# Kernel tuning notes

Measured on AMD Instinct MI355X. Metric: run time of the kernel, lower is better.

## Reference

```python
import jax, jax.numpy as jnp
import numpy as np

N, E, F_IN, HID, HEADS, OUT = 50000, 800000, 128, 64, 4, 40


def gat_layer(x, src, dst, n, W, a_src, a_dst, b, heads, ch):
    # PyG GATConv: h = x @ W per head; e_ij = LeakyReLU(a_src.h_j + a_dst.h_i)
    h = (x @ W).reshape(n, heads, ch)
    al_s = jnp.einsum('nhc,hc->nh', h, a_src)  # source-side logit term
    al_d = jnp.einsum('nhc,hc->nh', h, a_dst)  # target-side logit term
    e = jax.nn.leaky_relu(al_s[src] + al_d[dst], negative_slope=0.2)  # [E,H]
    m = jax.ops.segment_max(e, dst, num_segments=n)  # stable softmax per target node
    e = jnp.exp(e - m[dst])
    s = jax.ops.segment_sum(e, dst, num_segments=n)
    alpha = e / s[dst]  # [E,H]
    out = jax.ops.segment_sum(h[src] * alpha[:, :, None], dst, num_segments=n)  # [n,H,C]
    return out.reshape(n, heads * ch) + b


def gat_forward(x, src, dst, W0, as0, ad0, b0, W1, as1, ad1, b1, W2, as2, ad2, b2):
    n = x.shape[0]
    x = jax.nn.elu(gat_layer(x, src, dst, n, W0, as0, ad0, b0, HEADS, HID))
    x = jax.nn.elu(gat_layer(x, src, dst, n, W1, as1, ad1, b1, HEADS, HID))
    x = gat_layer(x, src, dst, n, W2, as2, ad2, b2, 1, OUT)
    return jax.nn.log_softmax(x, axis=1)


def setup_inputs() -> dict:
    key = jax.random.key(0)
    ks = jax.random.split(key, 16)
    x = jax.random.normal(ks[0], (N, F_IN), dtype=jnp.float32)
    edge_index = jax.random.randint(ks[1], (2, E), 0, N, dtype=jnp.int64)
    g = lambda k, sh: jax.random.normal(k, sh, dtype=jnp.float32) * (1.0 / np.sqrt(sh[0]))
    d_hid = HID * HEADS
    return {
        'x': x, 'edge_index': edge_index,
        'W0': g(ks[2], (F_IN, d_hid)), 'as0': g(ks[3], (HEADS, HID)), 'ad0': g(ks[4], (HEADS, HID)), 'b0': jnp.zeros((d_hid,), jnp.float32),
        'W1': g(ks[5], (d_hid, d_hid)), 'as1': g(ks[6], (HEADS, HID)), 'ad1': g(ks[7], (HEADS, HID)), 'b1': jnp.zeros((d_hid,), jnp.float32),
        'W2': g(ks[8], (d_hid, OUT)), 'as2': g(ks[9], (1, OUT)), 'ad2': g(ks[10], (1, OUT)), 'b2': jnp.zeros((OUT,), jnp.float32),
    }


def reference(x, edge_index, W0, as0, ad0, b0, W1, as1, ad1, b1, W2, as2, ad2, b2):
    n = x.shape[0]
    loops = jnp.arange(n, dtype=edge_index.dtype)  # PyG add_self_loops=True
    src = jnp.concatenate([edge_index[0], loops])
    dst = jnp.concatenate([edge_index[1], loops])
    return gat_forward(x, src, dst, W0, as0, ad0, b0, W1, as1, ad1, b1, W2, as2, ad2, b2)
```

## Files before the change

kernel.cpp:

```cpp
#include <hip/hip_runtime.h>
#include <hip/hip_fp16.h>
#include <math.h>

#define NODES 50000
#define NEDGES 800000
#define TOT_E (NEDGES + NODES)
#define SCAN_B 256
#define SCAN_NB ((NODES + SCAN_B - 1) / SCAN_B)

typedef __attribute__((ext_vector_type(8))) _Float16 half8v;
typedef __attribute__((ext_vector_type(4))) float f32x4;

union U2H { uint u; __half2 h; };

static __device__ __forceinline__ float lrelu(float z) {
  return z > 0.f ? z : 0.2f * z;
}
static __device__ __forceinline__ ushort f2h(float f) {
  __half h = __float2half_rn(f);
  return *reinterpret_cast<ushort*>(&h);
}
static __device__ __forceinline__ void wave_lds_fence() {
  __builtin_amdgcn_wave_barrier();
  asm volatile("s_waitcnt lgkmcnt(0)" ::: "memory");
  __builtin_amdgcn_sched_barrier(0);
}

static __device__ __forceinline__ void packB_one(const float* __restrict__ W,
    ushort* __restrict__ Bp, int N, int NF, int idx) {
  int i = idx & 7;
  int lane = (idx >> 3) & 63;
  int rem = idx >> 9;
  int nf = rem % NF;
  int kf = rem / NF;
  int k = kf * 32 + (lane >> 4) * 8 + i;
  int col = nf * 16 + (lane & 15);
  float v = (col < N) ? W[(size_t)k * N + col] : 0.f;
  Bp[idx] = f2h(v);
}

__global__ __launch_bounds__(256) void k_setup(const int* __restrict__ dst,
    int* __restrict__ counts, const float* __restrict__ x, ushort* __restrict__ xb0,
    const float* __restrict__ W0, ushort* __restrict__ Bp0,
    const float* __restrict__ W1, ushort* __restrict__ Bp1,
    const float* __restrict__ W2, ushort* __restrict__ Bp2) {
  int gb = blockIdx.x;
  int tid = threadIdx.x;
  if (gb < 2048) {
    int stride = 2048 * 256;
    for (int i = gb * 256 + tid; i < TOT_E; i += stride) {
      int d = (i < NEDGES) ? dst[i] : (i - NEDGES);
      atomicAdd(&counts[d], 1);
    }
  } else if (gb < 4048) {
    int total4 = NODES * 128 / 4;
    int stride = 2000 * 256;
    for (int i = (gb - 2048) * 256 + tid; i < total4; i += stride) {
      float4 v = *(const float4*)&x[i * 4];
      ushort4 o;
      o.x = f2h(v.x); o.y = f2h(v.y); o.z = f2h(v.z); o.w = f2h(v.w);
      *(ushort4*)&xb0[i * 4] = o;
    }
  } else {
    int b = gb - 4048;
    int stride = 48 * 256;
    int base = b * 256 + tid;
    for (int idx = base; idx < 4 * 16 * 512; idx += stride) packB_one(W0, Bp0, 256, 16, idx);
    for (int idx = base; idx < 8 * 16 * 512; idx += stride) packB_one(W1, Bp1, 256, 16, idx);
    for (int idx = base; idx < 8 * 3 * 512; idx += stride)  packB_one(W2, Bp2, 40, 3, idx);
  }
}

__global__ __launch_bounds__(SCAN_B) void k_scan_red(const int* __restrict__ counts,
                                                     int* __restrict__ bsum) {
  __shared__ int sm[SCAN_B];
  int idx = blockIdx.x * SCAN_B + threadIdx.x;
  int v = (idx < NODES) ? counts[idx] : 0;
  sm[threadIdx.x] = v;
  __syncthreads();
  for (int off = SCAN_B / 2; off > 0; off >>= 1) {
    if (threadIdx.x < off) sm[threadIdx.x] += sm[threadIdx.x + off];
    __syncthreads();
  }
  if (threadIdx.x == 0) bsum[blockIdx.x] = sm[0];
}

__global__ __launch_bounds__(256) void k_scan_part(const int* __restrict__ bsum,
                                                   int* __restrict__ bpre) {
  __shared__ int sm[256];
  int tid = threadIdx.x;
  int v = (tid < SCAN_NB) ? bsum[tid] : 0;
  sm[tid] = v;
  __syncthreads();
  for (int off = 1; off < 256; off <<= 1) {
    int t = (tid >= off) ? sm[tid - off] : 0;
    __syncthreads();
    sm[tid] += t;
    __syncthreads();
  }
  if (tid < SCAN_NB) bpre[tid] = sm[tid] - v;
}

__global__ __launch_bounds__(SCAN_B) void k_scan_emit(const int* __restrict__ counts,
    const int* __restrict__ bpre, int* __restrict__ offs, int* __restrict__ cur) {
  __shared__ int sm[SCAN_B];
  int idx = blockIdx.x * SCAN_B + threadIdx.x;
  int tid = threadIdx.x;
  int v = (idx < NODES) ? counts[idx] : 0;
  sm[tid] = v;
  __syncthreads();
  for (int off = 1; off < SCAN_B; off <<= 1) {
    int t = (tid >= off) ? sm[tid - off] : 0;
    __syncthreads();
    sm[tid] += t;
    __syncthreads();
  }
  int base = bpre[blockIdx.x];
  int excl = base + sm[tid] - v;
  if (idx < NODES) { offs[idx] = excl; cur[idx] = excl; }
  if (idx == NODES - 1) offs[NODES] = excl + v;
}

__global__ void k_scatter(const int* __restrict__ src, const int* __restrict__ dst,
                          int* __restrict__ cur, int* __restrict__ ssrc) {
  int stride = gridDim.x * blockDim.x;
  for (int i = blockIdx.x * blockDim.x + threadIdx.x; i < TOT_E; i += stride) {
    int s, d;
    if (i < NEDGES) { s = src[i]; d = dst[i]; } else { s = i - NEDGES; d = s; }
    int pos = atomicAdd(&cur[d], 1);
    ssrc[pos] = s;
  }
}

template<int KF, int NFW, int CG, int HEADS, int NF_TOT>
__global__ __launch_bounds__(256, 2) void k_gemm_reg(
    const ushort* __restrict__ A, const ushort* __restrict__ Bp,
    ushort* __restrict__ H, const float* __restrict__ a_s, const float* __restrict__ a_d,
    float* __restrict__ al_s, float* __restrict__ al_d, int M, int N, int K) {
  int wib = threadIdx.x >> 6;
  int lane = threadIdx.x & 63;
  int lg = lane >> 4;
  int lr = lane & 15;
  int cg, strip0, sstride;
  if (CG == 4) { cg = wib; strip0 = blockIdx.x; sstride = gridDim.x; }
  else { cg = 0; strip0 = blockIdx.x * 4 + wib; sstride = gridDim.x * 4; }

  half8v b[KF][NFW];
#pragma unroll
  for (int kf = 0; kf < KF; ++kf)
#pragma unroll
    for (int n = 0; n < NFW; ++n)
      b[kf][n] = *(const half8v*)(Bp + ((size_t)(kf * NF_TOT + cg * NFW + n) * 64 + lane) * 8);

  float asc[NFW], adc[NFW];
#pragma unroll
  for (int n = 0; n < NFW; ++n) {
    int col = (cg * NFW + n) * 16 + lr;
    bool ok = col < N;
    asc[n] = ok ? a_s[col] : 0.f;
    adc[n] = ok ? a_d[col] : 0.f;
  }

  int nstrips = M >> 4;
  for (int strip = strip0; strip < nstrips; strip += sstride) {
    const ushort* arow = A + (size_t)(strip * 16 + lr) * K + lg * 8;
    half8v a[KF];
#pragma unroll
    for (int kf = 0; kf < KF; ++kf) a[kf] = *(const half8v*)(arow + kf * 32);
    f32x4 acc[NFW];
#pragma unroll
    for (int n = 0; n < NFW; ++n) acc[n] = (f32x4){0.f, 0.f, 0.f, 0.f};
#pragma unroll
    for (int kf = 0; kf < KF; ++kf)
#pragma unroll
      for (int n = 0; n < NFW; ++n)
        acc[n] = __builtin_amdgcn_mfma_f32_16x16x32_f16(a[kf], b[kf][n], acc[n], 0, 0, 0);

#pragma unroll
    for (int n = 0; n < NFW; ++n) {
      int col = (cg * NFW + n) * 16 + lr;
      if (col < N) {
#pragma unroll
        for (int r = 0; r < 4; ++r) {
          int row = strip * 16 + lg * 4 + r;
          H[(size_t)row * N + col] = f2h(acc[n][r]);
        }
      }
    }

    float ps[4], pd[4];
#pragma unroll
    for (int r = 0; r < 4; ++r) {
      float s = 0.f, d = 0.f;
#pragma unroll
      for (int n = 0; n < NFW; ++n) {
        s += acc[n][r] * asc[n];
        d += acc[n][r] * adc[n];
      }
      ps[r] = s; pd[r] = d;
    }
#pragma unroll
    for (int off = 1; off <= 8; off <<= 1)
#pragma unroll
      for (int t = 0; t < 4; ++t) {
        ps[t] += __shfl_xor(ps[t], off);
        pd[t] += __shfl_xor(pd[t], off);
      }
    if (lr < 4) {
      int row = strip * 16 + lg * 4 + lr;
      if (HEADS == 4) {
        al_s[row * 4 + cg] = ps[lr];
        al_d[row * 4 + cg] = pd[lr];
      } else {
        al_s[row] = ps[lr];
        al_d[row] = pd[lr];
      }
    }
  }
}

__global__ __launch_bounds__(256) void k_agg4(const ushort* __restrict__ hb,
    const float* __restrict__ al_s, const float* __restrict__ al_d,
    const int* __restrict__ offs, const int* __restrict__ ssrc,
    const float* __restrict__ bias, ushort* __restrict__ outb) {
  __shared__ uint s_sv[8][32];
  __shared__ uint s_al[8][4][33];
  int hw = threadIdx.x >> 5;
  int node = (blockIdx.x * 256 + threadIdx.x) >> 5;
  if (node >= NODES) return;
  int l = threadIdx.x & 31;
  int beg = offs[node], end = offs[node + 1];
  float4 ald4 = *(const float4*)&al_d[node * 4];

  float m[4] = {-1e30f, -1e30f, -1e30f, -1e30f};
  for (int i = beg + l; i < end; i += 32) {
    int sv = ssrc[i];
    float4 a4 = *(const float4*)&al_s[sv * 4];
    m[0] = fmaxf(m[0], lrelu(a4.x + ald4.x));
    m[1] = fmaxf(m[1], lrelu(a4.y + ald4.y));
    m[2] = fmaxf(m[2], lrelu(a4.z + ald4.z));
    m[3] = fmaxf(m[3], lrelu(a4.w + ald4.w));
  }
#pragma unroll
  for (int off = 1; off <= 16; off <<= 1) {
#pragma unroll
    for (int h = 0; h < 4; ++h) m[h] = fmaxf(m[h], __shfl_xor(m[h], off));
  }

  int hh = l >> 3;
  uint clb = (uint)l * 8;
  float sacc[4] = {0.f, 0.f, 0.f, 0.f};
  __half2 z2 = __float2half2_rn(0.f);
  __half2 accA[4] = {z2, z2, z2, z2};
  __half2 accB[4] = {z2, z2, z2, z2};

  for (int cb = beg; cb < end; cb += 32) {
    int cnt = min(32, end - cb);
    wave_lds_fence();
    if (l < cnt) {
      uint sv = (uint)ssrc[cb + l];
      float4 a4 = *(const float4*)&al_s[sv * 4];
      float t0 = __expf(lrelu(a4.x + ald4.x) - m[0]);
      float t1 = __expf(lrelu(a4.y + ald4.y) - m[1]);
      float t2 = __expf(lrelu(a4.z + ald4.z) - m[2]);
      float t3 = __expf(lrelu(a4.w + ald4.w) - m[3]);
      sacc[0] += t0; sacc[1] += t1; sacc[2] += t2; sacc[3] += t3;
      U2H p0, p1, p2, p3;
      p0.h = __float2half2_rn(t0); p1.h = __float2half2_rn(t1);
      p2.h = __float2half2_rn(t2); p3.h = __float2half2_rn(t3);
      s_sv[hw][l] = sv;
      s_al[hw][0][l] = p0.u; s_al[hw][1][l] = p1.u;
      s_al[hw][2][l] = p2.u; s_al[hw][3][l] = p3.u;
    }
    wave_lds_fence();
    int e = 0;
    for (; e + 3 < cnt; e += 4) {
      uint sv0 = s_sv[hw][e],     sv1 = s_sv[hw][e + 1];
      uint sv2 = s_sv[hw][e + 2], sv3 = s_sv[hw][e + 3];
      U2H a0, a1, a2, a3;
      a0.u = s_al[hw][hh][e];     a1.u = s_al[hw][hh][e + 1];
      a2.u = s_al[hw][hh][e + 2]; a3.u = s_al[hw][hh][e + 3];
      uint4 hv0 = *(const uint4*)(hb + ((sv0 << 8) + clb));
      uint4 hv1 = *(const uint4*)(hb + ((sv1 << 8) + clb));
      uint4 hv2 = *(const uint4*)(hb + ((sv2 << 8) + clb));
      uint4 hv3 = *(const uint4*)(hb + ((sv3 << 8) + clb));
      U2H v;
      v.u = hv0.x; accA[0] = __hfma2(a0.h, v.h, accA[0]);
      v.u = hv0.y; accA[1] = __hfma2(a0.h, v.h, accA[1]);
      v.u = hv0.z; accA[2] = __hfma2(a0.h, v.h, accA[2]);
      v.u = hv0.w; accA[3] = __hfma2(a0.h, v.h, accA[3]);
      v.u = hv1.x; accB[0] = __hfma2(a1.h, v.h, accB[0]);
      v.u = hv1.y; accB[1] = __hfma2(a1.h, v.h, accB[1]);
      v.u = hv1.z; accB[2] = __hfma2(a1.h, v.h, accB[2]);
      v.u = hv1.w; accB[3] = __hfma2(a1.h, v.h, accB[3]);
      v.u = hv2.x; accA[0] = __hfma2(a2.h, v.h, accA[0]);
      v.u = hv2.y; accA[1] = __hfma2(a2.h, v.h, accA[1]);
      v.u = hv2.z; accA[2] = __hfma2(a2.h, v.h, accA[2]);
      v.u = hv2.w; accA[3] = __hfma2(a2.h, v.h, accA[3]);
      v.u = hv3.x; accB[0] = __hfma2(a3.h, v.h, accB[0]);
      v.u = hv3.y; accB[1] = __hfma2(a3.h, v.h, accB[1]);
      v.u = hv3.z; accB[2] = __hfma2(a3.h, v.h, accB[2]);
      v.u = hv3.w; accB[3] = __hfma2(a3.h, v.h, accB[3]);
    }
    for (; e < cnt; ++e) {
      uint sv = s_sv[hw][e];
      U2H a0; a0.u = s_al[hw][hh][e];
      uint4 hv = *(const uint4*)(hb + ((sv << 8) + clb));
      U2H v;
      v.u = hv.x; accA[0] = __hfma2(a0.h, v.h, accA[0]);
      v.u = hv.y; accA[1] = __hfma2(a0.h, v.h, accA[1]);
      v.u = hv.z; accA[2] = __hfma2(a0.h, v.h, accA[2]);
      v.u = hv.w; accA[3] = __hfma2(a0.h, v.h, accA[3]);
    }
  }
#pragma unroll
  for (int off = 1; off <= 16; off <<= 1) {
#pragma unroll
    for (int h = 0; h < 4; ++h) sacc[h] += __shfl_xor(sacc[h], off);
  }
  float invs = 1.f / sacc[hh];
  ushort4 ores[2];
#pragma unroll
  for (int j = 0; j < 4; ++j) {
    U2H t; t.h = __hadd2(accA[j], accB[j]);
    float lo = __low2float(t.h) * invs + bias[l * 8 + j * 2];
    float hi = __high2float(t.h) * invs + bias[l * 8 + j * 2 + 1];
    lo = lo > 0.f ? lo : __expf(lo) - 1.f;
    hi = hi > 0.f ? hi : __expf(hi) - 1.f;
    ((ushort*)ores)[j * 2]     = f2h(lo);
    ((ushort*)ores)[j * 2 + 1] = f2h(hi);
  }
  *(ushort4*)(outb + (size_t)node * 256 + l * 8)     = ores[0];
  *(ushort4*)(outb + (size_t)node * 256 + l * 8 + 4) = ores[1];
}

__global__ __launch_bounds__(256) void k_agg1(const ushort* __restrict__ hb,
    const float* __restrict__ al_s, const float* __restrict__ al_d,
    const int* __restrict__ offs, const int* __restrict__ ssrc,
    const float* __restrict__ bias, float* __restrict__ out) {
  __shared__ uint s_sv[8][32];
  __shared__ uint s_al[8][32];
  int hw = threadIdx.x >> 5;
  int node = (blockIdx.x * 256 + threadIdx.x) >> 5;
  if (node >= NODES) return;
  int l = threadIdx.x & 31;
  int beg = offs[node], end = offs[node + 1];
  float ald = al_d[node];

  float m = -1e30f;
  for (int i = beg + l; i < end; i += 32)
    m = fmaxf(m, lrelu(al_s[ssrc[i]] + ald));
#pragma unroll
  for (int off = 1; off <= 16; off <<= 1) m = fmaxf(m, __shfl_xor(m, off));

  int p = l >> 4;
  int cq = l & 15;
  bool act = cq < 10;
  uint cqb = (uint)cq * 4;
  float sacc = 0.f;
  __half2 z2 = __float2half2_rn(0.f);
  __half2 accA[2] = {z2, z2};
  __half2 accB[2] = {z2, z2};
  for (int cb = beg; cb < end; cb += 32) {
    int cnt = min(32, end - cb);
    wave_lds_fence();
    if (l < cnt) {
      uint sv = (uint)ssrc[cb + l];
      float t = __expf(lrelu(al_s[sv] + ald) - m);
      sacc += t;
      U2H pk; pk.h = __float2half2_rn(t);
      s_sv[hw][l] = sv;
      s_al[hw][l] = pk.u;
    }
    wave_lds_fence();
    int e = p;
    for (; e + 6 < cnt; e += 8) {
      uint sv0 = s_sv[hw][e],     sv1 = s_sv[hw][e + 2];
      uint sv2 = s_sv[hw][e + 4], sv3 = s_sv[hw][e + 6];
      U2H a0, a1, a2, a3;
      a0.u = s_al[hw][e];     a1.u = s_al[hw][e + 2];
      a2.u = s_al[hw][e + 4]; a3.u = s_al[hw][e + 6];
      if (act) {
        uint2 hv0 = *(const uint2*)(hb + (sv0 * 40u + cqb));
        uint2 hv1 = *(const uint2*)(hb + (sv1 * 40u + cqb));
        uint2 hv2 = *(const uint2*)(hb + (sv2 * 40u + cqb));
        uint2 hv3 = *(const uint2*)(hb + (sv3 * 40u + cqb));
        U2H v;
        v.u = hv0.x; accA[0] = __hfma2(a0.h, v.h, accA[0]);
        v.u = hv0.y; accA[1] = __hfma2(a0.h, v.h, accA[1]);
        v.u = hv1.x; accB[0] = __hfma2(a1.h, v.h, accB[0]);
        v.u = hv1.y; accB[1] = __hfma2(a1.h, v.h, accB[1]);
        v.u = hv2.x; accA[0] = __hfma2(a2.h, v.h, accA[0]);
        v.u = hv2.y; accA[1] = __hfma2(a2.h, v.h, accA[1]);
        v.u = hv3.x; accB[0] = __hfma2(a3.h, v.h, accB[0]);
        v.u = hv3.y; accB[1] = __hfma2(a3.h, v.h, accB[1]);
      }
    }
    for (; e < cnt; e += 2) {
      uint sv = s_sv[hw][e];
      U2H a0; a0.u = s_al[hw][e];
      if (act) {
        uint2 hv = *(const uint2*)(hb + (sv * 40u + cqb));
        U2H v;
        v.u = hv.x; accA[0] = __hfma2(a0.h, v.h, accA[0]);
        v.u = hv.y; accA[1] = __hfma2(a0.h, v.h, accA[1]);
      }
    }
  }
#pragma unroll
  for (int off = 1; off <= 16; off <<= 1) sacc += __shfl_xor(sacc, off);
  float invs = 1.f / sacc;
  float vv[4];
#pragma unroll
  for (int j = 0; j < 2; ++j) {
    U2H t; t.h = __hadd2(accA[j], accB[j]);
    U2H o; o.u = __shfl_xor(t.u, 16);
    t.h = __hadd2(t.h, o.h);
    vv[j * 2]     = __low2float(t.h) * invs;
    vv[j * 2 + 1] = __high2float(t.h) * invs;
  }
  float mm = -1e30f;
  if (act) {
#pragma unroll
    for (int j = 0; j < 4; ++j) {
      vv[j] += bias[cq * 4 + j];
      mm = fmaxf(mm, vv[j]);
    }
  }
#pragma unroll
  for (int off = 1; off <= 8; off <<= 1) mm = fmaxf(mm, __shfl_xor(mm, off));
  float se = 0.f;
  if (act) {
#pragma unroll
    for (int j = 0; j < 4; ++j) se += __expf(vv[j] - mm);
  }
#pragma unroll
  for (int off = 1; off <= 8; off <<= 1) se += __shfl_xor(se, off);
  if (act && p == 0) {
    float lse = mm + __logf(se);
    float4 o;
    o.x = vv[0] - lse; o.y = vv[1] - lse; o.z = vv[2] - lse; o.w = vv[3] - lse;
    *(float4*)&out[(size_t)node * 40 + cq * 4] = o;
  }
}

extern "C" void kernel_launch(void* const* d_in, const int* in_sizes, int n_in,
                              void* d_out, int out_size, void* d_ws, size_t ws_size,
                              hipStream_t stream) {
  const float* x   = (const float*)d_in[0];
  const int*   ei  = (const int*)d_in[1];
  const float* W0  = (const float*)d_in[2];
  const float* as0 = (const float*)d_in[3];
  const float* ad0 = (const float*)d_in[4];
  const float* b0  = (const float*)d_in[5];
  const float* W1  = (const float*)d_in[6];
  const float* as1 = (const float*)d_in[7];
  const float* ad1 = (const float*)d_in[8];
  const float* b1  = (const float*)d_in[9];
  const float* W2  = (const float*)d_in[10];
  const float* as2 = (const float*)d_in[11];
  const float* ad2 = (const float*)d_in[12];
  const float* b2  = (const float*)d_in[13];
  float* out = (float*)d_out;

  char* p = (char*)d_ws;
  auto take = [&](size_t bytes) {
    char* q = p;
    p += (bytes + 255) & ~(size_t)255;
    return (void*)q;
  };
  ushort* xb0 = (ushort*)take((size_t)NODES * 128 * 2);
  ushort* xb1 = (ushort*)take((size_t)NODES * 256 * 2);
  ushort* xb2 = (ushort*)take((size_t)NODES * 256 * 2);
  ushort* hb  = (ushort*)take((size_t)NODES * 256 * 2);
  float* als  = (float*)take((size_t)NODES * 4 * 4);
  float* ald  = (float*)take((size_t)NODES * 4 * 4);
  int* ssrc   = (int*)take((size_t)TOT_E * 4);
  int* offs   = (int*)take((size_t)(NODES + 1) * 4);
  int* cur    = (int*)take((size_t)NODES * 4);
  int* cnt    = (int*)take((size_t)NODES * 4);
  int* bsum   = (int*)take((size_t)SCAN_NB * 4);
  int* bpre   = (int*)take((size_t)SCAN_NB * 4);
  ushort* Bp0 = (ushort*)take((size_t)4 * 16 * 512 * 2);
  ushort* Bp1 = (ushort*)take((size_t)8 * 16 * 512 * 2);
  ushort* Bp2 = (ushort*)take((size_t)8 * 3 * 512 * 2);

  hipMemsetAsync(cnt, 0, (size_t)NODES * 4, stream);
  k_setup<<<4096, 256, 0, stream>>>(ei + NEDGES, cnt, x, xb0, W0, Bp0, W1, Bp1, W2, Bp2);
  k_scan_red<<<SCAN_NB, SCAN_B, 0, stream>>>(cnt, bsum);
  k_scan_part<<<1, 256, 0, stream>>>(bsum, bpre);
  k_scan_emit<<<SCAN_NB, SCAN_B, 0, stream>>>(cnt, bpre, offs, cur);
  k_scatter<<<2048, 256, 0, stream>>>(ei, ei + NEDGES, cur, ssrc);

  int nab = (NODES * 32 + 255) / 256;

  k_gemm_reg<4, 4, 4, 4, 16><<<512, 256, 0, stream>>>(xb0, Bp0, hb, as0, ad0, als, ald, NODES, 256, 128);
  k_agg4<<<nab, 256, 0, stream>>>(hb, als, ald, offs, ssrc, b0, xb1);

  k_gemm_reg<8, 4, 4, 4, 16><<<512, 256, 0, stream>>>(xb1, Bp1, hb, as1, ad1, als, ald, NODES, 256, 256);
  k_agg4<<<nab, 256, 0, stream>>>(hb, als, ald, offs, ssrc, b1, xb2);

  k_gemm_reg<8, 3, 1, 1, 3><<<512, 256, 0, stream>>>(xb2, Bp2, hb, as2, ad2, als, ald, NODES, 40, 256);
  k_agg1<<<nab, 256, 0, stream>>>(hb, als, ald, offs, ssrc, b2, out);
}
```

Measured before the change: 304.3 us.

## Split 4-head aggregation into edge-stats pass and channel-group gather kernel

Replaces the fused per-node aggregation with two kernels. The first computes the softmax max, the per-edge exp weights and the inverse sums, and writes packed (src index | fp16 weight) words per head to a global buffer. The second assigns 16 lanes per node per 32-channel group, spread across 8 blocks, and gathers 4-byte slices of h with nontemporal loads of the packed weights. The aim is more parallelism and no LDS syncs in the gather, at the cost of an extra pass writing about 13.6MB of per-edge data, re-reading the edge list once per channel group, and narrower 4-byte gathers in place of 16-byte ones.

```diff
diff --git a/kernel.cpp b/kernel.cpp
--- a/kernel.cpp
+++ b/kernel.cpp
@@ -219,13 +219,10 @@
   }
 }
 
-__global__ __launch_bounds__(256) void k_agg4(const ushort* __restrict__ hb,
+__global__ __launch_bounds__(256) void k_stats4(
     const float* __restrict__ al_s, const float* __restrict__ al_d,
     const int* __restrict__ offs, const int* __restrict__ ssrc,
-    const float* __restrict__ bias, ushort* __restrict__ outb) {
-  __shared__ uint s_sv[8][32];
-  __shared__ uint s_al[8][4][33];
-  int hw = threadIdx.x >> 5;
+    uint* __restrict__ alp, float* __restrict__ snorm) {
   int node = (blockIdx.x * 256 + threadIdx.x) >> 5;
   if (node >= NODES) return;
   int l = threadIdx.x & 31;
@@ -247,91 +244,84 @@
     for (int h = 0; h < 4; ++h) m[h] = fmaxf(m[h], __shfl_xor(m[h], off));
   }
 
-  int hh = l >> 3;
-  uint clb = (uint)l * 8;
-  float sacc[4] = {0.f, 0.f, 0.f, 0.f};
+  float s0 = 0.f, s1 = 0.f, s2 = 0.f, s3 = 0.f;
+  for (int i = beg + l; i < end; i += 32) {
+    uint sv = (uint)ssrc[i];
+    float4 a4 = *(const float4*)&al_s[sv * 4];
+    float t0 = __expf(lrelu(a4.x + ald4.x) - m[0]);
+    float t1 = __expf(lrelu(a4.y + ald4.y) - m[1]);
+    float t2 = __expf(lrelu(a4.z + ald4.z) - m[2]);
+    float t3 = __expf(lrelu(a4.w + ald4.w) - m[3]);
+    s0 += t0; s1 += t1; s2 += t2; s3 += t3;
+    alp[i]             = sv | ((uint)f2h(t0) << 16);
+    alp[TOT_E + i]     = sv | ((uint)f2h(t1) << 16);
+    alp[2 * TOT_E + i] = sv | ((uint)f2h(t2) << 16);
+    alp[3 * TOT_E + i] = sv | ((uint)f2h(t3) << 16);
+  }
+#pragma unroll
+  for (int off = 1; off <= 16; off <<= 1) {
+    s0 += __shfl_xor(s0, off); s1 += __shfl_xor(s1, off);
+    s2 += __shfl_xor(s2, off); s3 += __shfl_xor(s3, off);
+  }
+  if (l == 0) {
+    float4 inv = make_float4(1.f / s0, 1.f / s1, 1.f / s2, 1.f / s3);
+    *(float4*)&snorm[node * 4] = inv;
+  }
+}
+
+__global__ __launch_bounds__(256) void k_gather4(const ushort* __restrict__ hb,
+    const uint* __restrict__ alp, const float* __restrict__ snorm,
+    const int* __restrict__ offs, const float* __restrict__ bias,
+    ushort* __restrict__ outb) {
+  int bid = blockIdx.x;
+  int cg = bid & 7;
+  int chunk = bid >> 3;
+  int g = threadIdx.x >> 4;
+  int l = threadIdx.x & 15;
+  int node = chunk * 16 + g;
+  if (node >= NODES) return;
+  int beg = offs[node], end = offs[node + 1];
+  int hh = cg >> 1;
+  const uint* alph = alp + (size_t)hh * TOT_E;
+  uint choff = ((uint)cg << 5) + ((uint)l << 1);
+
   __half2 z2 = __float2half2_rn(0.f);
-  __half2 accA[4] = {z2, z2, z2, z2};
-  __half2 accB[4] = {z2, z2, z2, z2};
-
-  for (int cb = beg; cb < end; cb += 32) {
-    int cnt = min(32, end - cb);
-    wave_lds_fence();
-    if (l < cnt) {
-      uint sv = (uint)ssrc[cb + l];
-      float4 a4 = *(const float4*)&al_s[sv * 4];
-      float t0 = __expf(lrelu(a4.x + ald4.x) - m[0]);
-      float t1 = __expf(lrelu(a4.y + ald4.y) - m[1]);
-      float t2 = __expf(lrelu(a4.z + ald4.z) - m[2]);
-      float t3 = __expf(lrelu(a4.w + ald4.w) - m[3]);
-      sacc[0] += t0; sacc[1] += t1; sacc[2] += t2; sacc[3] += t3;
-      U2H p0, p1, p2, p3;
-      p0.h = __float2half2_rn(t0); p1.h = __float2half2_rn(t1);
-      p2.h = __float2half2_rn(t2); p3.h = __float2half2_rn(t3);
-      s_sv[hw][l] = sv;
-      s_al[hw][0][l] = p0.u; s_al[hw][1][l] = p1.u;
-      s_al[hw][2][l] = p2.u; s_al[hw][3][l] = p3.u;
-    }
-    wave_lds_fence();
-    int e = 0;
-    for (; e + 3 < cnt; e += 4) {
-      uint sv0 = s_sv[hw][e],     sv1 = s_sv[hw][e + 1];
-      uint sv2 = s_sv[hw][e + 2], sv3 = s_sv[hw][e + 3];
-      U2H a0, a1, a2, a3;
-      a0.u = s_al[hw][hh][e];     a1.u = s_al[hw][hh][e + 1];
-      a2.u = s_al[hw][hh][e + 2]; a3.u = s_al[hw][hh][e + 3];
-      uint4 hv0 = *(const uint4*)(hb + ((sv0 << 8) + clb));
-      uint4 hv1 = *(const uint4*)(hb + ((sv1 << 8) + clb));
-      uint4 hv2 = *(const uint4*)(hb + ((sv2 << 8) + clb));
-      uint4 hv3 = *(const uint4*)(hb + ((sv3 << 8) + clb));
-      U2H v;
-      v.u = hv0.x; accA[0] = __hfma2(a0.h, v.h, accA[0]);
-      v.u = hv0.y; accA[1] = __hfma2(a0.h, v.h, accA[1]);
-      v.u = hv0.z; accA[2] = __hfma2(a0.h, v.h, accA[2]);
-      v.u = hv0.w; accA[3] = __hfma2(a0.h, v.h, accA[3]);
-      v.u = hv1.x; accB[0] = __hfma2(a1.h, v.h, accB[0]);
-      v.u = hv1.y; accB[1] = __hfma2(a1.h, v.h, accB[1]);
-      v.u = hv1.z; accB[2] = __hfma2(a1.h, v.h, accB[2]);
-      v.u = hv1.w; accB[3] = __hfma2(a1.h, v.h, accB[3]);
-      v.u = hv2.x; accA[0] = __hfma2(a2.h, v.h, accA[0]);
-      v.u = hv2.y; accA[1] = __hfma2(a2.h, v.h, accA[1]);
-      v.u = hv2.z; accA[2] = __hfma2(a2.h, v.h, accA[2]);
-      v.u = hv2.w; accA[3] = __hfma2(a2.h, v.h, accA[3]);
-      v.u = hv3.x; accB[0] = __hfma2(a3.h, v.h, accB[0]);
-      v.u = hv3.y; accB[1] = __hfma2(a3.h, v.h, accB[1]);
-      v.u = hv3.z; accB[2] = __hfma2(a3.h, v.h, accB[2]);
-      v.u = hv3.w; accB[3] = __hfma2(a3.h, v.h, accB[3]);
-    }
-    for (; e < cnt; ++e) {
-      uint sv = s_sv[hw][e];
-      U2H a0; a0.u = s_al[hw][hh][e];
-      uint4 hv = *(const uint4*)(hb + ((sv << 8) + clb));
-      U2H v;
-      v.u = hv.x; accA[0] = __hfma2(a0.h, v.h, accA[0]);
-      v.u = hv.y; accA[1] = __hfma2(a0.h, v.h, accA[1]);
-      v.u = hv.z; accA[2] = __hfma2(a0.h, v.h, accA[2]);
-      v.u = hv.w; accA[3] = __hfma2(a0.h, v.h, accA[3]);
-    }
-  }
-#pragma unroll
-  for (int off = 1; off <= 16; off <<= 1) {
-#pragma unroll
-    for (int h = 0; h < 4; ++h) sacc[h] += __shfl_xor(sacc[h], off);
-  }
-  float invs = 1.f / sacc[hh];
-  ushort4 ores[2];
-#pragma unroll
-  for (int j = 0; j < 4; ++j) {
-    U2H t; t.h = __hadd2(accA[j], accB[j]);
-    float lo = __low2float(t.h) * invs + bias[l * 8 + j * 2];
-    float hi = __high2float(t.h) * invs + bias[l * 8 + j * 2 + 1];
-    lo = lo > 0.f ? lo : __expf(lo) - 1.f;
-    hi = hi > 0.f ? hi : __expf(hi) - 1.f;
-    ((ushort*)ores)[j * 2]     = f2h(lo);
-    ((ushort*)ores)[j * 2 + 1] = f2h(hi);
-  }
-  *(ushort4*)(outb + (size_t)node * 256 + l * 8)     = ores[0];
-  *(ushort4*)(outb + (size_t)node * 256 + l * 8 + 4) = ores[1];
+  __half2 accA = z2, accB = z2;
+  int i = beg;
+  for (; i + 3 < end; i += 4) {
+    uint u0 = __builtin_nontemporal_load(&alph[i]);
+    uint u1 = __builtin_nontemporal_load(&alph[i + 1]);
+    uint u2 = __builtin_nontemporal_load(&alph[i + 2]);
+    uint u3 = __builtin_nontemporal_load(&alph[i + 3]);
+    U2H v0, v1, v2, v3;
+    v0.u = *(const uint*)(hb + (((u0 & 0xFFFFu) << 8) + choff));
+    v1.u = *(const uint*)(hb + (((u1 & 0xFFFFu) << 8) + choff));
+    v2.u = *(const uint*)(hb + (((u2 & 0xFFFFu) << 8) + choff));
+    v3.u = *(const uint*)(hb + (((u3 & 0xFFFFu) << 8) + choff));
+    U2H a0, a1, a2, a3;
+    a0.u = (u0 >> 16) * 0x10001u;
+    a1.u = (u1 >> 16) * 0x10001u;
+    a2.u = (u2 >> 16) * 0x10001u;
+    a3.u = (u3 >> 16) * 0x10001u;
+    accA = __hfma2(a0.h, v0.h, accA);
+    accB = __hfma2(a1.h, v1.h, accB);
+    accA = __hfma2(a2.h, v2.h, accA);
+    accB = __hfma2(a3.h, v3.h, accB);
+  }
+  for (; i < end; ++i) {
+    uint u = __builtin_nontemporal_load(&alph[i]);
+    U2H v; v.u = *(const uint*)(hb + (((u & 0xFFFFu) << 8) + choff));
+    U2H a; a.u = (u >> 16) * 0x10001u;
+    accA = __hfma2(a.h, v.h, accA);
+  }
+  __half2 acc = __hadd2(accA, accB);
+  float invs = snorm[node * 4 + hh];
+  float lo = __low2float(acc) * invs + bias[(cg << 5) + l * 2];
+  float hi = __high2float(acc) * invs + bias[(cg << 5) + l * 2 + 1];
+  lo = lo > 0.f ? lo : __expf(lo) - 1.f;
+  hi = hi > 0.f ? hi : __expf(hi) - 1.f;
+  ushort2 o = make_ushort2(f2h(lo), f2h(hi));
+  *(ushort2*)(outb + (size_t)node * 256 + choff) = o;
 }
 
 __global__ __launch_bounds__(256) void k_agg1(const ushort* __restrict__ hb,
@@ -475,7 +465,9 @@
   ushort* hb  = (ushort*)take((size_t)NODES * 256 * 2);
   float* als  = (float*)take((size_t)NODES * 4 * 4);
   float* ald  = (float*)take((size_t)NODES * 4 * 4);
+  float* snorm= (float*)take((size_t)NODES * 4 * 4);
   int* ssrc   = (int*)take((size_t)TOT_E * 4);
+  uint* alp   = (uint*)take((size_t)4 * TOT_E * 4);
   int* offs   = (int*)take((size_t)(NODES + 1) * 4);
   int* cur    = (int*)take((size_t)NODES * 4);
   int* cnt    = (int*)take((size_t)NODES * 4);
@@ -492,14 +484,17 @@
   k_scan_emit<<<SCAN_NB, SCAN_B, 0, stream>>>(cnt, bpre, offs, cur);
   k_scatter<<<2048, 256, 0, stream>>>(ei, ei + NEDGES, cur, ssrc);
 
-  int nab = (NODES * 32 + 255) / 256;
+  int nsb = (NODES * 32 + 255) / 256;
+  int ngb = (NODES / 16) * 8;
 
   k_gemm_reg<4, 4, 4, 4, 16><<<512, 256, 0, stream>>>(xb0, Bp0, hb, as0, ad0, als, ald, NODES, 256, 128);
-  k_agg4<<<nab, 256, 0, stream>>>(hb, als, ald, offs, ssrc, b0, xb1);
+  k_stats4<<<nsb, 256, 0, stream>>>(als, ald, offs, ssrc, alp, snorm);
+  k_gather4<<<ngb, 256, 0, stream>>>(hb, alp, snorm, offs, b0, xb1);
 
   k_gemm_reg<8, 4, 4, 4, 16><<<512, 256, 0, stream>>>(xb1, Bp1, hb, as1, ad1, als, ald, NODES, 256, 256);
-  k_agg4<<<nab, 256, 0, stream>>>(hb, als, ald, offs, ssrc, b1, xb2);
+  k_stats4<<<nsb, 256, 0, stream>>>(als, ald, offs, ssrc, alp, snorm);
+  k_gather4<<<ngb, 256, 0, stream>>>(hb, alp, snorm, offs, b1, xb2);
 
   k_gemm_reg<8, 3, 1, 1, 3><<<512, 256, 0, stream>>>(xb2, Bp2, hb, as2, ad2, als, ald, NODES, 40, 256);
-  k_agg1<<<nab, 256, 0, stream>>>(hb, als, ald, offs, ssrc, b2, out);
-}
+  k_agg1<<<nsb, 256, 0, stream>>>(hb, als, ald, offs, ssrc, b2, out);
+}
```

New measurement: 467.9 us. +53.8%, slower.

## Aggregate raw features before projection in layer 0; fold attention vectors into W0

Applied to the files above, without the earlier changes.

Layer 0 now precomputes W0·a_src and W0·a_dst so the attention logits come straight from the 128-wide fp16 input. The per-head weighted aggregation then runs over 128-wide raw features instead of 256-wide projected ones, followed by a per-head MFMA GEMM that applies 1/sum normalisation, bias and ELU. This reorders aggregation and the linear map, which is valid because the map is linear. Separately, the scan reduce and partial-scan kernels merge through a last-block atomic, the logit computation is fused into the scan-emit launch, and the CSR source indices shrink to 16-bit. The GEMM in layer 0 now processes per-head aggregates (512 wide per node), so its work grows while the gather traffic shrinks.

```diff
diff --git a/kernel.cpp b/kernel.cpp
--- a/kernel.cpp
+++ b/kernel.cpp
@@ -7,6 +7,7 @@
 #define TOT_E (NEDGES + NODES)
 #define SCAN_B 256
 #define SCAN_NB ((NODES + SCAN_B - 1) / SCAN_B)
+#define ALOG_NB (NODES / 16)
 
 typedef __attribute__((ext_vector_type(8))) _Float16 half8v;
 typedef __attribute__((ext_vector_type(4))) float f32x4;
@@ -41,7 +42,9 @@
 
 __global__ __launch_bounds__(256) void k_setup(const int* __restrict__ dst,
     int* __restrict__ counts, const float* __restrict__ x, ushort* __restrict__ xb0,
-    const float* __restrict__ W0, ushort* __restrict__ Bp0,
+    const float* __restrict__ W0, ushort* __restrict__ Bq0,
+    float* __restrict__ Uu, float* __restrict__ Vv,
+    const float* __restrict__ as0, const float* __restrict__ ad0,
     const float* __restrict__ W1, ushort* __restrict__ Bp1,
     const float* __restrict__ W2, ushort* __restrict__ Bp2) {
   int gb = blockIdx.x;
@@ -61,19 +64,47 @@
       o.x = f2h(v.x); o.y = f2h(v.y); o.z = f2h(v.z); o.w = f2h(v.w);
       *(ushort4*)&xb0[i * 4] = o;
     }
-  } else {
+  } else if (gb < 4096) {
     int b = gb - 4048;
     int stride = 48 * 256;
     int base = b * 256 + tid;
-    for (int idx = base; idx < 4 * 16 * 512; idx += stride) packB_one(W0, Bp0, 256, 16, idx);
     for (int idx = base; idx < 8 * 16 * 512; idx += stride) packB_one(W1, Bp1, 256, 16, idx);
     for (int idx = base; idx < 8 * 3 * 512; idx += stride)  packB_one(W2, Bp2, 40, 3, idx);
-  }
-}
-
-__global__ __launch_bounds__(SCAN_B) void k_scan_red(const int* __restrict__ counts,
-                                                     int* __restrict__ bsum) {
+  } else if (gb < 4224) {
+    int idx = (gb - 4096) * 256 + tid;
+    int i = idx & 7;
+    int lane = (idx >> 3) & 63;
+    int rem = idx >> 9;
+    int nf = rem & 3;
+    int kf = (rem >> 2) & 3;
+    int h = rem >> 4;
+    int k = kf * 32 + (lane >> 4) * 8 + i;
+    int col = h * 64 + nf * 16 + (lane & 15);
+    Bq0[idx] = f2h(W0[(size_t)k * 256 + col]);
+  } else {
+    int idx = (gb - 4224) * 256 + tid;
+    if (idx < 512) {
+      int c = idx & 127;
+      int h = idx >> 7;
+      float su = 0.f, sv = 0.f;
+      const float* wr = &W0[(size_t)c * 256 + h * 64];
+      const float* ar = &as0[h * 64];
+      const float* dr = &ad0[h * 64];
+#pragma unroll 8
+      for (int j = 0; j < 64; ++j) {
+        su += wr[j] * ar[j];
+        sv += wr[j] * dr[j];
+      }
+      Uu[c * 4 + h] = su;
+      Vv[c * 4 + h] = sv;
+    }
+  }
+}
+
+__global__ __launch_bounds__(SCAN_B) void k_scan_red_part(const int* __restrict__ counts,
+    int* __restrict__ bsum, int* __restrict__ bpre, int* __restrict__ done) {
   __shared__ int sm[SCAN_B];
+  __shared__ int lastflag;
   int idx = blockIdx.x * SCAN_B + threadIdx.x;
   int v = (idx < NODES) ? counts[idx] : 0;
   sm[threadIdx.x] = v;
@@ -82,53 +113,245 @@
     if (threadIdx.x < off) sm[threadIdx.x] += sm[threadIdx.x + off];
     __syncthreads();
   }
-  if (threadIdx.x == 0) bsum[blockIdx.x] = sm[0];
-}
-
-__global__ __launch_bounds__(256) void k_scan_part(const int* __restrict__ bsum,
-                                                   int* __restrict__ bpre) {
-  __shared__ int sm[256];
+  if (threadIdx.x == 0) {
+    __hip_atomic_store(&bsum[blockIdx.x], sm[0], __ATOMIC_RELEASE, __HIP_MEMORY_SCOPE_AGENT);
+    int t = __hip_atomic_fetch_add(done, 1, __ATOMIC_ACQ_REL, __HIP_MEMORY_SCOPE_AGENT);
+    lastflag = (t == (int)gridDim.x - 1);
+  }
+  __syncthreads();
+  if (!lastflag) return;
   int tid = threadIdx.x;
-  int v = (tid < SCAN_NB) ? bsum[tid] : 0;
-  sm[tid] = v;
+  int b = (tid < SCAN_NB)
+      ? __hip_atomic_load(&bsum[tid], __ATOMIC_ACQUIRE, __HIP_MEMORY_SCOPE_AGENT) : 0;
+  __syncthreads();
+  sm[tid] = b;
   __syncthreads();
   for (int off = 1; off < 256; off <<= 1) {
-    int t = (tid >= off) ? sm[tid - off] : 0;
+    int t2 = (tid >= off) ? sm[tid - off] : 0;
     __syncthreads();
-    sm[tid] += t;
+    sm[tid] += t2;
     __syncthreads();
   }
-  if (tid < SCAN_NB) bpre[tid] = sm[tid] - v;
-}
-
-__global__ __launch_bounds__(SCAN_B) void k_scan_emit(const int* __restrict__ counts,
-    const int* __restrict__ bpre, int* __restrict__ offs, int* __restrict__ cur) {
-  __shared__ int sm[SCAN_B];
-  int idx = blockIdx.x * SCAN_B + threadIdx.x;
-  int tid = threadIdx.x;
-  int v = (idx < NODES) ? counts[idx] : 0;
-  sm[tid] = v;
-  __syncthreads();
-  for (int off = 1; off < SCAN_B; off <<= 1) {
-    int t = (tid >= off) ? sm[tid - off] : 0;
+  if (tid < SCAN_NB) bpre[tid] = sm[tid] - b;
+}
+
+__global__ __launch_bounds__(SCAN_B) void k_scan_emit_alog(const int* __restrict__ counts,
+    const int* __restrict__ bpre, int* __restrict__ offs, int* __restrict__ cur,
+    const ushort* __restrict__ xb0, const float* __restrict__ Uu,
+    const float* __restrict__ Vv, float* __restrict__ als, float* __restrict__ ald) {
+  if (blockIdx.x < SCAN_NB) {
+    __shared__ int sm[SCAN_B];
+    int idx = blockIdx.x * SCAN_B + threadIdx.x;
+    int tid = threadIdx.x;
+    int v = (idx < NODES) ? counts[idx] : 0;
+    sm[tid] = v;
     __syncthreads();
-    sm[tid] += t;
-    __syncthreads();
-  }
-  int base = bpre[blockIdx.x];
-  int excl = base + sm[tid] - v;
-  if (idx < NODES) { offs[idx] = excl; cur[idx] = excl; }
-  if (idx == NODES - 1) offs[NODES] = excl + v;
+    for (int off = 1; off < SCAN_B; off <<= 1) {
+      int t = (tid >= off) ? sm[tid - off] : 0;
+      __syncthreads();
+      sm[tid] += t;
+      __syncthreads();
+    }
+    int base = bpre[blockIdx.x];
+    int excl = base + sm[tid] - v;
+    if (idx < NODES) { offs[idx] = excl; cur[idx] = excl; }
+    if (idx == NODES - 1) offs[NODES] = excl + v;
+    return;
+  }
+  int node = ((blockIdx.x - SCAN_NB) * 256 + threadIdx.x) >> 4;
+  int l = threadIdx.x & 15;
+  float s4[4] = {0.f, 0.f, 0.f, 0.f};
+  float d4[4] = {0.f, 0.f, 0.f, 0.f};
+  uint4 raw = *(const uint4*)(xb0 + (size_t)node * 128 + l * 8);
+  const uint* rw = &raw.x;
+#pragma unroll
+  for (int w = 0; w < 4; ++w) {
+    U2H u; u.u = rw[w];
+    float x0 = __low2float(u.h), x1 = __high2float(u.h);
+    int c0 = l * 8 + w * 2;
+    float4 u0 = *(const float4*)&Uu[c0 * 4];
+    float4 u1 = *(const float4*)&Uu[(c0 + 1) * 4];
+    float4 v0 = *(const float4*)&Vv[c0 * 4];
+    float4 v1 = *(const float4*)&Vv[(c0 + 1) * 4];
+    s4[0] += x0 * u0.x + x1 * u1.x; s4[1] += x0 * u0.y + x1 * u1.y;
+    s4[2] += x0 * u0.z + x1 * u1.z; s4[3] += x0 * u0.w + x1 * u1.w;
+    d4[0] += x0 * v0.x + x1 * v1.x; d4[1] += x0 * v0.y + x1 * v1.y;
+    d4[2] += x0 * v0.z + x1 * v1.z; d4[3] += x0 * v0.w + x1 * v1.w;
+  }
+#pragma unroll
+  for (int off = 1; off <= 8; off <<= 1) {
+#pragma unroll
+    for (int h = 0; h < 4; ++h) {
+      s4[h] += __shfl_xor(s4[h], off);
+      d4[h] += __shfl_xor(d4[h], off);
+    }
+  }
+  if (l == 0) {
+    *(float4*)&als[node * 4] = make_float4(s4[0], s4[1], s4[2], s4[3]);
+    *(float4*)&ald[node * 4] = make_float4(d4[0], d4[1], d4[2], d4[3]);
+  }
 }
 
 __global__ void k_scatter(const int* __restrict__ src, const int* __restrict__ dst,
-                          int* __restrict__ cur, int* __restrict__ ssrc) {
+                          int* __restrict__ cur, ushort* __restrict__ ssrc) {
   int stride = gridDim.x * blockDim.x;
   for (int i = blockIdx.x * blockDim.x + threadIdx.x; i < TOT_E; i += stride) {
     int s, d;
     if (i < NEDGES) { s = src[i]; d = dst[i]; } else { s = i - NEDGES; d = s; }
     int pos = atomicAdd(&cur[d], 1);
-    ssrc[pos] = s;
+    ssrc[pos] = (ushort)s;
+  }
+}
+
+__global__ __launch_bounds__(256) void k_agg0(const ushort* __restrict__ xb0,
+    const float* __restrict__ al_s, const float* __restrict__ al_d,
+    const int* __restrict__ offs, const ushort* __restrict__ ssrc,
+    ushort* __restrict__ agg, float* __restrict__ snorm) {
+  __shared__ uint s_sv[8][32];
+  __shared__ uint2 s_al2[8][32];
+  int hw = threadIdx.x >> 5;
+  int node = (blockIdx.x * 256 + threadIdx.x) >> 5;
+  if (node >= NODES) return;
+  int l = threadIdx.x & 31;
+  int beg = offs[node], end = offs[node + 1];
+  float4 ald4 = *(const float4*)&al_d[node * 4];
+
+  float m[4] = {-1e30f, -1e30f, -1e30f, -1e30f};
+  for (int i = beg + l; i < end; i += 32) {
+    int sv = ssrc[i];
+    float4 a4 = *(const float4*)&al_s[sv * 4];
+    m[0] = fmaxf(m[0], lrelu(a4.x + ald4.x));
+    m[1] = fmaxf(m[1], lrelu(a4.y + ald4.y));
+    m[2] = fmaxf(m[2], lrelu(a4.z + ald4.z));
+    m[3] = fmaxf(m[3], lrelu(a4.w + ald4.w));
+  }
+#pragma unroll
+  for (int off = 1; off <= 16; off <<= 1) {
+#pragma unroll
+    for (int h = 0; h < 4; ++h) m[h] = fmaxf(m[h], __shfl_xor(m[h], off));
+  }
+
+  float sacc[4] = {0.f, 0.f, 0.f, 0.f};
+  __half2 z2 = __float2half2_rn(0.f);
+  __half2 accA[8] = {z2, z2, z2, z2, z2, z2, z2, z2};
+  __half2 accB[8] = {z2, z2, z2, z2, z2, z2, z2, z2};
+  uint clb = (uint)l * 4;
+
+  for (int cb = beg; cb < end; cb += 32) {
+    int cnt = min(32, end - cb);
+    wave_lds_fence();
+    if (l < cnt) {
+      uint sv = (uint)ssrc[cb + l];
+      float4 a4 = *(const float4*)&al_s[sv * 4];
+      float t0 = __expf(lrelu(a4.x + ald4.x) - m[0]);
+      float t1 = __expf(lrelu(a4.y + ald4.y) - m[1]);
+      float t2 = __expf(lrelu(a4.z + ald4.z) - m[2]);
+      float t3 = __expf(lrelu(a4.w + ald4.w) - m[3]);
+      sacc[0] += t0; sacc[1] += t1; sacc[2] += t2; sacc[3] += t3;
+      s_sv[hw][l] = sv;
+      s_al2[hw][l] = make_uint2((uint)f2h(t0) | ((uint)f2h(t1) << 16),
+                                (uint)f2h(t2) | ((uint)f2h(t3) << 16));
+    }
+    wave_lds_fence();
+    int e = 0;
+    for (; e + 3 < cnt; e += 4) {
+      uint sv0 = s_sv[hw][e],     sv1 = s_sv[hw][e + 1];
+      uint sv2 = s_sv[hw][e + 2], sv3 = s_sv[hw][e + 3];
+      uint2 w0 = s_al2[hw][e],     w1 = s_al2[hw][e + 1];
+      uint2 w2 = s_al2[hw][e + 2], w3 = s_al2[hw][e + 3];
+      uint2 hv0 = *(const uint2*)(xb0 + ((sv0 << 7) + clb));
+      uint2 hv1 = *(const uint2*)(xb0 + ((sv1 << 7) + clb));
+      uint2 hv2 = *(const uint2*)(xb0 + ((sv2 << 7) + clb));
+      uint2 hv3 = *(const uint2*)(xb0 + ((sv3 << 7) + clb));
+      U2H a, v;
+#define EDGE(ACC, W, HV)                                                      \
+      v.u = HV.x;                                                             \
+      a.u = (W.x & 0xFFFFu) * 0x10001u; ACC[0] = __hfma2(a.h, v.h, ACC[0]);   \
+      a.u = (W.x >> 16) * 0x10001u;     ACC[2] = __hfma2(a.h, v.h, ACC[2]);   \
+      a.u = (W.y & 0xFFFFu) * 0x10001u; ACC[4] = __hfma2(a.h, v.h, ACC[4]);   \
+      a.u = (W.y >> 16) * 0x10001u;     ACC[6] = __hfma2(a.h, v.h, ACC[6]);   \
+      v.u = HV.y;                                                             \
+      a.u = (W.x & 0xFFFFu) * 0x10001u; ACC[1] = __hfma2(a.h, v.h, ACC[1]);   \
+      a.u = (W.x >> 16) * 0x10001u;     ACC[3] = __hfma2(a.h, v.h, ACC[3]);   \
+      a.u = (W.y & 0xFFFFu) * 0x10001u; ACC[5] = __hfma2(a.h, v.h, ACC[5]);   \
+      a.u = (W.y >> 16) * 0x10001u;     ACC[7] = __hfma2(a.h, v.h, ACC[7]);
+      EDGE(accA, w0, hv0)
+      EDGE(accB, w1, hv1)
+      EDGE(accA, w2, hv2)
+      EDGE(accB, w3, hv3)
+    }
+    for (; e < cnt; ++e) {
+      uint sv = s_sv[hw][e];
+      uint2 w = s_al2[hw][e];
+      uint2 hv = *(const uint2*)(xb0 + ((sv << 7) + clb));
+      U2H a, v;
+      EDGE(accA, w, hv)
+    }
+#undef EDGE
+  }
+#pragma unroll
+  for (int off = 1; off <= 16; off <<= 1) {
+#pragma unroll
+    for (int h = 0; h < 4; ++h) sacc[h] += __shfl_xor(sacc[h], off);
+  }
+  if (l == 0) {
+    *(float4*)&snorm[node * 4] = make_float4(1.f / sacc[0], 1.f / sacc[1],
+                                             1.f / sacc[2], 1.f / sacc[3]);
+  }
+#pragma unroll
+  for (int h = 0; h < 4; ++h) {
+    U2H a0, a1;
+    a0.h = __hadd2(accA[h * 2], accB[h * 2]);
+    a1.h = __hadd2(accA[h * 2 + 1], accB[h * 2 + 1]);
+    *(uint2*)(agg + (size_t)node * 512 + h * 128 + clb) = make_uint2(a0.u, a1.u);
+  }
+}
+
+__global__ __launch_bounds__(256, 2) void k_gemm_post(const ushort* __restrict__ agg,
+    const ushort* __restrict__ Bq0, const float* __restrict__ snorm,
+    const float* __restrict__ bias, ushort* __restrict__ xb1) {
+  int h = threadIdx.x >> 6;
+  int lane = threadIdx.x & 63;
+  int lg = lane >> 4;
+  int lr = lane & 15;
+
+  half8v b[4][4];
+#pragma unroll
+  for (int kf = 0; kf < 4; ++kf)
+#pragma unroll
+    for (int n = 0; n < 4; ++n)
+      b[kf][n] = *(const half8v*)(Bq0 + (((size_t)(h * 4 + kf) * 4 + n) * 64 + lane) * 8);
+
+  int nstrips = NODES >> 4;
+  for (int strip = blockIdx.x; strip < nstrips; strip += gridDim.x) {
+    const ushort* arow = agg + (size_t)(strip * 16 + lr) * 512 + h * 128 + lg * 8;
+    half8v a[4];
+#pragma unroll
+    for (int kf = 0; kf < 4; ++kf) a[kf] = *(const half8v*)(arow + kf * 32);
+    f32x4 acc[4];
+#pragma unroll
+    for (int n = 0; n < 4; ++n) acc[n] = (f32x4){0.f, 0.f, 0.f, 0.f};
+#pragma unroll
+    for (int kf = 0; kf < 4; ++kf)
+#pragma unroll
+      for (int n = 0; n < 4; ++n)
+        acc[n] = __builtin_amdgcn_mfma_f32_16x16x32_f16(a[kf], b[kf][n], acc[n], 0, 0, 0);
+
+    float sn[4];
+#pragma unroll
+    for (int r = 0; r < 4; ++r) sn[r] = snorm[(strip * 16 + lg * 4 + r) * 4 + h];
+#pragma unroll
+    for (int n = 0; n < 4; ++n) {
+      int col = h * 64 + n * 16 + lr;
+      float bcol = bias[col];
+#pragma unroll
+      for (int r = 0; r < 4; ++r) {
+        int node = strip * 16 + lg * 4 + r;
+        float v = acc[n][r] * sn[r] + bcol;
+        v = v > 0.f ? v : __expf(v) - 1.f;
+        xb1[(size_t)node * 256 + col] = f2h(v);
+      }
+    }
   }
 }
 
@@ -221,7 +444,7 @@
 
 __global__ __launch_bounds__(256) void k_agg4(const ushort* __restrict__ hb,
     const float* __restrict__ al_s, const float* __restrict__ al_d,
-    const int* __restrict__ offs, const int* __restrict__ ssrc,
+    const int* __restrict__ offs, const ushort* __restrict__ ssrc,
     const float* __restrict__ bias, ushort* __restrict__ outb) {
   __shared__ uint s_sv[8][32];
   __shared__ uint s_al[8][4][33];
@@ -336,7 +559,7 @@
 
 __global__ __launch_bounds__(256) void k_agg1(const ushort* __restrict__ hb,
     const float* __restrict__ al_s, const float* __restrict__ al_d,
-    const int* __restrict__ offs, const int* __restrict__ ssrc,
+    const int* __restrict__ offs, const ushort* __restrict__ ssrc,
     const float* __restrict__ bias, float* __restrict__ out) {
   __shared__ uint s_sv[8][32];
   __shared__ uint s_al[8][32];
@@ -473,29 +696,35 @@
   ushort* xb1 = (ushort*)take((size_t)NODES * 256 * 2);
   ushort* xb2 = (ushort*)take((size_t)NODES * 256 * 2);
   ushort* hb  = (ushort*)take((size_t)NODES * 256 * 2);
+  ushort* agg = xb2;
   float* als  = (float*)take((size_t)NODES * 4 * 4);
   float* ald  = (float*)take((size_t)NODES * 4 * 4);
-  int* ssrc   = (int*)take((size_t)TOT_E * 4);
+  float* snorm= (float*)take((size_t)NODES * 4 * 4);
+  ushort* ssrc= (ushort*)take((size_t)TOT_E * 2);
   int* offs   = (int*)take((size_t)(NODES + 1) * 4);
   int* cur    = (int*)take((size_t)NODES * 4);
-  int* cnt    = (int*)take((size_t)NODES * 4);
+  int* cnt    = (int*)take((size_t)(NODES + 64) * 4);
+  int* done   = cnt + NODES;
   int* bsum   = (int*)take((size_t)SCAN_NB * 4);
   int* bpre   = (int*)take((size_t)SCAN_NB * 4);
-  ushort* Bp0 = (ushort*)take((size_t)4 * 16 * 512 * 2);
+  float* Uu   = (float*)take((size_t)128 * 4 * 4);
+  float* Vv   = (float*)take((size_t)128 * 4 * 4);
+  ushort* Bq0 = (ushort*)take((size_t)4 * 4 * 4 * 512 * 2);
   ushort* Bp1 = (ushort*)take((size_t)8 * 16 * 512 * 2);
   ushort* Bp2 = (ushort*)take((size_t)8 * 3 * 512 * 2);
 
-  hipMemsetAsync(cnt, 0, (size_t)NODES * 4, stream);
-  k_setup<<<4096, 256, 0, stream>>>(ei + NEDGES, cnt, x, xb0, W0, Bp0, W1, Bp1, W2, Bp2);
-  k_scan_red<<<SCAN_NB, SCAN_B, 0, stream>>>(cnt, bsum);
-  k_scan_part<<<1, 256, 0, stream>>>(bsum, bpre);
-  k_scan_emit<<<SCAN_NB, SCAN_B, 0, stream>>>(cnt, bpre, offs, cur);
-  k_scatter<<<2048, 256, 0, stream>>>(ei, ei + NEDGES, cur, ssrc);
+  hipMemsetAsync(cnt, 0, (size_t)(NODES + 64) * 4, stream);
+  k_setup<<<4226, 256, 0, stream>>>(ei + NEDGES, cnt, x, xb0, W0, Bq0, Uu, Vv,
+                                    as0, ad0, W1, Bp1, W2, Bp2);
+  k_scan_red_part<<<SCAN_NB, SCAN_B, 0, stream>>>(cnt, bsum, bpre, done);
+  k_scan_emit_alog<<<SCAN_NB + ALOG_NB, SCAN_B, 0, stream>>>(cnt, bpre, offs, cur,
+                                                             xb0, Uu, Vv, als, ald);
+  k_scatter<<<4096, 256, 0, stream>>>(ei, ei + NEDGES, cur, ssrc);
 
   int nab = (NODES * 32 + 255) / 256;
 
-  k_gemm_reg<4, 4, 4, 4, 16><<<512, 256, 0, stream>>>(xb0, Bp0, hb, as0, ad0, als, ald, NODES, 256, 128);
-  k_agg4<<<nab, 256, 0, stream>>>(hb, als, ald, offs, ssrc, b0, xb1);
+  k_agg0<<<nab, 256, 0, stream>>>(xb0, als, ald, offs, ssrc, agg, snorm);
+  k_gemm_post<<<512, 256, 0, stream>>>(agg, Bq0, snorm, b0, xb1);
 
   k_gemm_reg<8, 4, 4, 4, 16><<<512, 256, 0, stream>>>(xb1, Bp1, hb, as1, ad1, als, ald, NODES, 256, 256);
   k_agg4<<<nab, 256, 0, stream>>>(hb, als, ald, offs, ssrc, b1, xb2);
```

New measurement: 303.9 us. No clear change (-0.2%).
